# Optimization experiments

Hardware: AMD Instinct MI355X
Metric: run time of the kernel (lower is better)

## Reference

```python
import jax, jax.numpy as jnp
import numpy as np

V, D, R, E, B, T, S = 32000, 512, 512, 512, 32, 64, 64  # vocab, embed, rnn, enc, batch, trg_len, src_len


def setup_inputs() -> dict:
    key = jax.random.key(0)
    ks = jax.random.split(key, 16)
    s = 0.02
    return {
        "trg": jax.random.randint(ks[0], (B, T), 0, V),
        "enc_outputs": jax.random.normal(ks[1], (B, S, E), jnp.float32),
        "init_hidden": jax.random.normal(ks[2], (1, B, R), jnp.float32),
        "src_mask": jnp.ones((B, S), jnp.float32),
        "emb_W": jax.random.normal(ks[3], (V, D), jnp.float32) * s,   # embedding table, tied with logits weight
        "W_ih": jax.random.normal(ks[4], (3 * R, D + D), jnp.float32) * s,  # GRU input weights (input = emb + input_feed)
        "W_hh": jax.random.normal(ks[5], (3 * R, R), jnp.float32) * s,
        "b_ih": jnp.zeros((3 * R,), jnp.float32),
        "b_hh": jnp.zeros((3 * R,), jnp.float32),
        "W_a": jax.random.normal(ks[6], (R, E), jnp.float32) * s,     # attention 'general': enc_proj = enc @ W_a^T
        "W_h": jax.random.normal(ks[7], (D, R), jnp.float32) * s,     # outputs_fn='sum' projections to o_size=D
        "b_h": jnp.zeros((D,), jnp.float32),
        "W_c": jax.random.normal(ks[8], (D, E), jnp.float32) * s,
        "b_c": jnp.zeros((D,), jnp.float32),
        "b_logits": jnp.zeros((V,), jnp.float32),
    }


def _decode(trg, enc_outputs, init_hidden, src_mask, emb_W, W_ih, W_hh, b_ih, b_hh,
            W_a, W_h, b_h, W_c, b_c, b_logits):
    # teacher forcing (eval mode, sampling=0): input token at step i is trg[:, i]
    emb = emb_W[trg]                              # [B,T,D]
    enc_proj = jnp.einsum('bse,re->bsr', enc_outputs, W_a)  # precompute_enc_projections
    neg = jnp.asarray(-1e9, emb.dtype)

    def step(carry, e_i):
        h, o_prev = carry                          # h:[B,R], o_prev:[B,D] (input feed)
        x = jnp.concatenate([e_i, o_prev], -1)     # [B, 2D]
        gx = x @ W_ih.T + b_ih                     # [B, 3R]
        gh = h @ W_hh.T + b_hh
        gx_r, gx_z, gx_n = jnp.split(gx, 3, axis=-1)
        gh_r, gh_z, gh_n = jnp.split(gh, 3, axis=-1)
        r = jax.nn.sigmoid(gx_r + gh_r)
        z = jax.nn.sigmoid(gx_z + gh_z)
        n = jnp.tanh(gx_n + r * gh_n)
        h_new = (1.0 - z) * n + z * h              # GRU cell (torch gate order r,z,n)
        # attention ('general'): score = enc_proj . query
        scores = jnp.einsum('bsr,br->bs', enc_proj, h_new)
        scores = jnp.where(src_mask > 0, scores, neg)
        attn = jax.nn.softmax(scores, axis=-1)
        context = jnp.einsum('bs,bse->be', attn, enc_outputs)   # [B,E]
        o = jnp.tanh(h_new @ W_h.T + b_h + context @ W_c.T + b_c)  # sum + tanh
        logits = o @ emb_W.T + b_logits            # tied projection [B,V]
        return (h_new, o), logits

    h0 = init_hidden[0]                            # [B,R]
    o0 = jnp.zeros((B, emb_W.shape[1]), emb.dtype)
    _, logits = jax.lax.scan(step, (h0, o0), jnp.swapaxes(emb, 0, 1))
    return jnp.swapaxes(logits, 0, 1)              # [B,T,V]


def reference(trg, enc_outputs, init_hidden, src_mask, emb_W, W_ih, W_hh, b_ih, b_hh,
              W_a, W_h, b_h, W_c, b_c, b_logits):
    return _decode(trg, enc_outputs, init_hidden, src_mask, emb_W, W_ih, W_hh,
                   b_ih, b_hh, W_a, W_h, b_h, W_c, b_c, b_logits)
```

## Files before the change

kernel.cpp:

```cpp
#include <hip/hip_runtime.h>

#define V_ 32000
#define D_ 512
#define R_ 512
#define E_ 512
#define B_ 32
#define T_ 64
#define S_ 64
#define BT_ (B_ * T_)
#define G3_ (3 * R_)

typedef _Float16 f16;
typedef _Float16 f16x2 __attribute__((ext_vector_type(2)));
typedef _Float16 f16x8 __attribute__((ext_vector_type(8)));
typedef __bf16 bf16x8 __attribute__((ext_vector_type(8)));
typedef float f32x4 __attribute__((ext_vector_type(4)));

#define PAIR(v, i) (f16x2){(v)[2*(i)], (v)[2*(i)+1]}

__device__ __forceinline__ float fdot2_(f16x2 a, f16x2 b, float c) {
    return __builtin_amdgcn_fdot2(a, b, c, false);
}
__device__ __forceinline__ float sigmoidf_(float x) {
    return 1.0f / (1.0f + __expf(-x));
}

__global__ __launch_bounds__(256) void k_convert_bf16(const float* __restrict__ src,
                                                      __bf16* __restrict__ dst, int n8) {
    int i = blockIdx.x * 256 + threadIdx.x;
    if (i >= n8) return;
    float4 a = *(const float4*)&src[(size_t)i * 8];
    float4 b = *(const float4*)&src[(size_t)i * 8 + 4];
    bf16x8 o;
    o[0] = (__bf16)a.x; o[1] = (__bf16)a.y; o[2] = (__bf16)a.z; o[3] = (__bf16)a.w;
    o[4] = (__bf16)b.x; o[5] = (__bf16)b.y; o[6] = (__bf16)b.z; o[7] = (__bf16)b.w;
    *(bf16x8*)&dst[(size_t)i * 8] = o;
}

__global__ __launch_bounds__(256) void k_convert_f16(const float* __restrict__ src,
                                                     f16* __restrict__ dst, int n8) {
    int i = blockIdx.x * 256 + threadIdx.x;
    if (i >= n8) return;
    float4 a = *(const float4*)&src[(size_t)i * 8];
    float4 b = *(const float4*)&src[(size_t)i * 8 + 4];
    f16x8 o;
    o[0] = (f16)a.x; o[1] = (f16)a.y; o[2] = (f16)a.z; o[3] = (f16)a.w;
    o[4] = (f16)b.x; o[5] = (f16)b.y; o[6] = (f16)b.z; o[7] = (f16)b.w;
    *(f16x8*)&dst[(size_t)i * 8] = o;
}

__global__ __launch_bounds__(256) void k_gather_emb(const int* __restrict__ trg,
                                                    const __bf16* __restrict__ embW,
                                                    __bf16* __restrict__ dst) {
    int id = blockIdx.x * 256 + threadIdx.x;
    int bt = id >> 6, c = id & 63;
    int tok = trg[bt];
    *(uint4*)&dst[(size_t)bt * 512 + c * 8] = *(const uint4*)&embW[(size_t)tok * 512 + c * 8];
}

__global__ __launch_bounds__(256) void k_gemm_bf16(const __bf16* __restrict__ A,
                                                   const __bf16* __restrict__ B,
                                                   const float* __restrict__ bias,
                                                   float* __restrict__ out,
                                                   int M, int N, int K, int lda, int ldb,
                                                   int mode) {
    __shared__ __bf16 lA[128 * 40];
    __shared__ __bf16 lB[128 * 40];
    const int Mt = M >> 7;
    const int mt = blockIdx.x % Mt, nt = blockIdx.x / Mt;
    const int m0 = mt << 7, n0 = nt << 7;
    const int tid = threadIdx.x;
    const int w = tid >> 6, ln = tid & 63;
    const int wm = w >> 1, wn = w & 1;

    f32x4 acc[4][4];
#pragma unroll
    for (int mi = 0; mi < 4; ++mi)
#pragma unroll
        for (int ni = 0; ni < 4; ++ni) acc[mi][ni] = (f32x4){0.f, 0.f, 0.f, 0.f};

    const int k0 = (ln >> 4) * 8, rr = ln & 15;

    for (int kk = 0; kk < K; kk += 32) {
        __syncthreads();
#pragma unroll
        for (int p = 0; p < 2; ++p) {
            int i = p * 256 + tid;
            int r = i >> 2, q = i & 3;
            *(uint4*)&lA[r * 40 + q * 8] = *(const uint4*)&A[(size_t)(m0 + r) * lda + kk + q * 8];
            *(uint4*)&lB[r * 40 + q * 8] = *(const uint4*)&B[(size_t)(n0 + r) * ldb + kk + q * 8];
        }
        __syncthreads();
        bf16x8 af[4], bf[4];
#pragma unroll
        for (int mi = 0; mi < 4; ++mi) af[mi] = *(bf16x8*)&lA[(wm * 64 + mi * 16 + rr) * 40 + k0];
#pragma unroll
        for (int ni = 0; ni < 4; ++ni) bf[ni] = *(bf16x8*)&lB[(wn * 64 + ni * 16 + rr) * 40 + k0];
#pragma unroll
        for (int mi = 0; mi < 4; ++mi)
#pragma unroll
            for (int ni = 0; ni < 4; ++ni)
                acc[mi][ni] = __builtin_amdgcn_mfma_f32_16x16x32_bf16(af[mi], bf[ni], acc[mi][ni], 0, 0, 0);
    }

    const int rq = ln >> 4;
#pragma unroll
    for (int mi = 0; mi < 4; ++mi) {
#pragma unroll
        for (int ni = 0; ni < 4; ++ni) {
            int col = n0 + wn * 64 + ni * 16 + rr;
            float bv = bias ? bias[col] : 0.f;
#pragma unroll
            for (int reg = 0; reg < 4; ++reg) {
                int row = m0 + wm * 64 + mi * 16 + rq * 4 + reg;
                float v = acc[mi][ni][reg] + bv;
                if (mode == 0) {
                    out[(size_t)row * N + col] = v;
                } else {
                    int bb = row >> 6, tt = row & 63;
                    out[((size_t)tt * G3_ + col) * B_ + bb] = v;
                }
            }
        }
    }
}

__global__ __launch_bounds__(256) void k_pack_gates(const float* __restrict__ Wih,
                                                    const float* __restrict__ Whh,
                                                    f16* __restrict__ Wg) {
    int idx = blockIdx.x * 256 + threadIdx.x;
    int j3 = idx >> 10, k = idx & 1023;
    float v = (k < 512) ? Wih[(size_t)j3 * 1024 + 512 + k] : Whh[(size_t)j3 * 512 + (k - 512)];
    Wg[idx] = (f16)v;
}
__global__ __launch_bounds__(256) void k_pack_ewT(const float* __restrict__ ew, f16* __restrict__ ewT) {
    int idx = blockIdx.x * 256 + threadIdx.x;
    int b = idx >> 15, d = (idx >> 6) & 511, s = idx & 63;
    ewT[idx] = (f16)ew[((size_t)b * 64 + s) * 512 + d];
}
__global__ __launch_bounds__(256) void k_init_state(const float* __restrict__ init_h,
                                                    f16* __restrict__ x16,
                                                    float* __restrict__ hbuf) {
    int idx = blockIdx.x * 256 + threadIdx.x;
    int b = idx >> 10, k = idx & 1023;
    if (k < 512) {
        x16[idx] = (f16)0.f;
    } else {
        float v = init_h[(size_t)b * 512 + (k - 512)];
        x16[idx] = (f16)v;
        hbuf[(size_t)b * 512 + (k - 512)] = v;
    }
}

__global__ __launch_bounds__(256) void k_stepA(
    const f16* __restrict__ Wg, const float* __restrict__ gp, const float* __restrict__ bhh,
    const f16* __restrict__ x_in, f16* __restrict__ x_out,
    const float* __restrict__ h_in, float* __restrict__ h_out) {
    __shared__ __align__(16) f16 x2l[32 * 1032];
    const int tid = threadIdx.x;
    const int wgid = blockIdx.x;
    const int bA = tid & 31;
    const int half = (tid >> 5) & 1;
    const int jl = tid >> 6;
    const int j = wgid * 4 + jl;

#pragma unroll
    for (int i = 0; i < 16; ++i) {
        int f = tid + i * 256;
        int row = f >> 7, col = f & 127;
        *(uint4*)(x2l + row * 1032 + col * 8) = *(const uint4*)(x_in + (size_t)f * 8);
    }
    __syncthreads();

    const f16* xb = x2l + bA * 1032 + half * 512;
    const f16* wr = Wg + (size_t)(j) * 1024 + half * 512;
    const f16* wz = Wg + (size_t)(512 + j) * 1024 + half * 512;
    const f16* wn = Wg + (size_t)(1024 + j) * 1024 + half * 512;
    float ar = 0.f, az = 0.f, an = 0.f;
#pragma unroll 4
    for (int c = 0; c < 64; ++c) {
        f16x8 xv = *(const f16x8*)(xb + c * 8);
        f16x8 wrv = *(const f16x8*)(wr + c * 8);
        f16x8 wzv = *(const f16x8*)(wz + c * 8);
        f16x8 wnv = *(const f16x8*)(wn + c * 8);
#pragma unroll
        for (int q = 0; q < 4; ++q) {
            f16x2 xp = PAIR(xv, q);
            ar = fdot2_(xp, PAIR(wrv, q), ar);
            az = fdot2_(xp, PAIR(wzv, q), az);
            an = fdot2_(xp, PAIR(wnv, q), an);
        }
    }
    float aro = __shfl_xor(ar, 32);
    float azo = __shfl_xor(az, 32);
    float ano = __shfl_xor(an, 32);
    float gr = gp[(size_t)j * 32 + bA];
    float gz = gp[(size_t)(512 + j) * 32 + bA];
    float gn = gp[(size_t)(1024 + j) * 32 + bA];
    float rpre = gr + bhh[j] + ar + aro;
    float zpre = gz + bhh[512 + j] + az + azo;
    float r = sigmoidf_(rpre);
    float z = sigmoidf_(zpre);
    float gxn = gn + (half ? ano : an);
    float ghn = bhh[1024 + j] + (half ? an : ano);
    float n = tanhf(gxn + r * ghn);
    float hp = h_in[(size_t)bA * 512 + j];
    float hnew = (1.f - z) * n + z * hp;
    if (half == 0) {
        h_out[(size_t)bA * 512 + j] = hnew;
        x_out[(size_t)bA * 1024 + 512 + j] = (f16)hnew;
    }
}

__global__ __launch_bounds__(256) void k_stepB(
    const f16* __restrict__ whf16, const f16* __restrict__ epf16, const f16* __restrict__ encWcT,
    const float* __restrict__ mask, const float* __restrict__ bh, const float* __restrict__ bc,
    f16* __restrict__ x_out, __bf16* __restrict__ obf, int t) {
    __shared__ __align__(16) f16 hl16[512];
    __shared__ float sc_[64];
    __shared__ float s_af[64];
    __shared__ f16x2 a2l[32];
    const int tid = threadIdx.x;
    const int b = blockIdx.x >> 1, dh = blockIdx.x & 1;

    if (tid < 64) {
        *(uint4*)(hl16 + tid * 8) = *(const uint4*)(x_out + (size_t)b * 1024 + 512 + tid * 8);
    }
    __syncthreads();

    {
        int s = tid >> 2, q = tid & 3;
        const f16* ep = epf16 + ((size_t)(b * 64 + s)) * 512 + q * 128;
        const f16* hh = hl16 + q * 128;
        float a = 0.f;
#pragma unroll
        for (int c = 0; c < 16; ++c) {
            f16x8 ev = *(const f16x8*)(ep + c * 8);
            f16x8 xv = *(const f16x8*)(hh + c * 8);
#pragma unroll
            for (int qq = 0; qq < 4; ++qq) a = fdot2_(PAIR(ev, qq), PAIR(xv, qq), a);
        }
        a += __shfl_xor(a, 1);
        a += __shfl_xor(a, 2);
        if (q == 0) sc_[s] = a;
    }
    __syncthreads();
    if (tid < 64) {
        float s = sc_[tid];
        s = (mask[b * 64 + tid] > 0.f) ? s : -1e9f;
        float m = s;
#pragma unroll
        for (int d = 1; d < 64; d <<= 1) m = fmaxf(m, __shfl_xor(m, d));
        float e = __expf(s - m);
        float sum = e;
#pragma unroll
        for (int d = 1; d < 64; d <<= 1) sum += __shfl_xor(sum, d);
        s_af[tid] = e / sum;
    }
    __syncthreads();
    if (tid < 32) {
        a2l[tid] = (f16x2){(f16)s_af[2 * tid], (f16)s_af[2 * tid + 1]};
    }
    __syncthreads();
    {
        const int d = dh * 256 + tid;
        float u = bh[d] + bc[d];
        const f16* wrow = whf16 + (size_t)d * 512;
#pragma unroll 8
        for (int c = 0; c < 64; ++c) {
            f16x8 wv = *(const f16x8*)(wrow + c * 8);
            f16x8 xv = *(const f16x8*)(hl16 + c * 8);
#pragma unroll
            for (int qq = 0; qq < 4; ++qq) u = fdot2_(PAIR(wv, qq), PAIR(xv, qq), u);
        }
        const f16* ew = encWcT + ((size_t)b * 512 + d) * 64;
#pragma unroll
        for (int c = 0; c < 8; ++c) {
            f16x8 ev = *(const f16x8*)(ew + c * 8);
#pragma unroll
            for (int qq = 0; qq < 4; ++qq) u = fdot2_(PAIR(ev, qq), a2l[c * 4 + qq], u);
        }
        float o = tanhf(u);
        obf[((size_t)b * 64 + t) * 512 + d] = (__bf16)o;
        x_out[(size_t)b * 1024 + d] = (f16)o;
    }
}

extern "C" void kernel_launch(void* const* d_in, const int* in_sizes, int n_in,
                              void* d_out, int out_size, void* d_ws, size_t ws_size,
                              hipStream_t stream) {
    const int* trg = (const int*)d_in[0];
    const float* enc = (const float*)d_in[1];
    const float* init_h = (const float*)d_in[2];
    const float* mask = (const float*)d_in[3];
    const float* embW = (const float*)d_in[4];
    const float* Wih = (const float*)d_in[5];
    const float* Whh = (const float*)d_in[6];
    const float* bih = (const float*)d_in[7];
    const float* bhh = (const float*)d_in[8];
    const float* Wa = (const float*)d_in[9];
    const float* Wh = (const float*)d_in[10];
    const float* bh = (const float*)d_in[11];
    const float* Wc = (const float*)d_in[12];
    const float* bc = (const float*)d_in[13];
    const float* blog = (const float*)d_in[14];
    float* out = (float*)d_out;

    char* w = (char*)d_ws;
    auto alloc = [&](size_t bytes) { char* p = w; w += (bytes + 255) & ~(size_t)255; return p; };
    __bf16* embW_bf = (__bf16*)alloc((size_t)V_ * D_ * 2);
    __bf16* Wih_bf  = (__bf16*)alloc((size_t)G3_ * 1024 * 2);
    __bf16* Wa_bf   = (__bf16*)alloc((size_t)R_ * E_ * 2);
    __bf16* Wc_bf   = (__bf16*)alloc((size_t)D_ * E_ * 2);
    __bf16* enc_bf  = (__bf16*)alloc((size_t)BT_ * E_ * 2);
    __bf16* emb_bf  = (__bf16*)alloc((size_t)BT_ * D_ * 2);
    float* gxe      = (float*)alloc((size_t)T_ * G3_ * B_ * 4);
    float* encproj  = (float*)alloc((size_t)BT_ * R_ * 4);
    float* encWc    = (float*)alloc((size_t)BT_ * D_ * 4);
    f16* Wg         = (f16*)alloc((size_t)G3_ * 1024 * 2);
    f16* whf16      = (f16*)alloc((size_t)512 * 512 * 2);
    f16* epf16      = (f16*)alloc((size_t)BT_ * 512 * 2);
    f16* encWcT     = (f16*)alloc((size_t)32 * 512 * 64 * 2);
    f16* x16        = (f16*)alloc((size_t)2 * 32 * 1024 * 2);
    float* hbuf     = (float*)alloc((size_t)2 * 32 * 512 * 4);
    __bf16* o_bf    = (__bf16*)alloc((size_t)BT_ * D_ * 2);

    k_convert_bf16<<<(V_ * D_ / 8 + 255) / 256, 256, 0, stream>>>(embW, embW_bf, V_ * D_ / 8);
    k_convert_bf16<<<(G3_ * 1024 / 8 + 255) / 256, 256, 0, stream>>>(Wih, Wih_bf, G3_ * 1024 / 8);
    k_convert_bf16<<<(R_ * E_ / 8 + 255) / 256, 256, 0, stream>>>(Wa, Wa_bf, R_ * E_ / 8);
    k_convert_bf16<<<(D_ * E_ / 8 + 255) / 256, 256, 0, stream>>>(Wc, Wc_bf, D_ * E_ / 8);
    k_convert_bf16<<<(BT_ * E_ / 8 + 255) / 256, 256, 0, stream>>>(enc, enc_bf, BT_ * E_ / 8);

    k_gather_emb<<<(BT_ * 64) / 256, 256, 0, stream>>>(trg, embW_bf, emb_bf);

    k_gemm_bf16<<<(BT_ / 128) * (G3_ / 128), 256, 0, stream>>>(
        emb_bf, Wih_bf, bih, gxe, BT_, G3_, 512, 512, 1024, 1);

    k_gemm_bf16<<<(BT_ / 128) * (R_ / 128), 256, 0, stream>>>(
        enc_bf, Wa_bf, nullptr, encproj, BT_, R_, 512, 512, 512, 0);
    k_gemm_bf16<<<(BT_ / 128) * (D_ / 128), 256, 0, stream>>>(
        enc_bf, Wc_bf, nullptr, encWc, BT_, D_, 512, 512, 512, 0);

    k_pack_gates<<<(G3_ * 1024) / 256, 256, 0, stream>>>(Wih, Whh, Wg);
    k_convert_f16<<<(512 * 512 / 8 + 255) / 256, 256, 0, stream>>>(Wh, whf16, 512 * 512 / 8);
    k_convert_f16<<<(BT_ * 512 / 8 + 255) / 256, 256, 0, stream>>>(encproj, epf16, BT_ * 512 / 8);
    k_pack_ewT<<<(32 * 512 * 64) / 256, 256, 0, stream>>>(encWc, encWcT);
    k_init_state<<<(32 * 1024) / 256, 256, 0, stream>>>(init_h, x16, hbuf);

    for (int t = 0; t < T_; ++t) {
        const f16* x_in = x16 + (size_t)(t & 1) * 32 * 1024;
        f16* x_out = x16 + (size_t)((t + 1) & 1) * 32 * 1024;
        const float* h_in = hbuf + (size_t)(t & 1) * 32 * 512;
        float* h_out = hbuf + (size_t)((t + 1) & 1) * 32 * 512;
        k_stepA<<<128, 256, 0, stream>>>(Wg, gxe + (size_t)t * G3_ * B_, bhh,
                                         x_in, x_out, h_in, h_out);
        k_stepB<<<64, 256, 0, stream>>>(whf16, epf16, encWcT, mask, bh, bc,
                                        x_out, o_bf, t);
    }

    k_gemm_bf16<<<(BT_ / 128) * (V_ / 128), 256, 0, stream>>>(
        o_bf, embW_bf, blog, out, BT_, V_, 512, 512, 512, 0);
}
```

Measured before the change: 1.613 ms.

## Fuse setup conversions into one kernel, gather embeddings in GEMM, use direct-to-LDS loads

```diff
diff --git a/kernel.cpp b/kernel.cpp
--- a/kernel.cpp
+++ b/kernel.cpp
@@ -18,6 +18,9 @@
 
 #define PAIR(v, i) (f16x2){(v)[2*(i)], (v)[2*(i)+1]}
 
+typedef __attribute__((address_space(3))) char lds_char;
+typedef __attribute__((address_space(1))) const char glob_char;
+
 __device__ __forceinline__ float fdot2_(f16x2 a, f16x2 b, float c) {
     return __builtin_amdgcn_fdot2(a, b, c, false);
 }
@@ -25,47 +28,91 @@
     return 1.0f / (1.0f + __expf(-x));
 }
 
-__global__ __launch_bounds__(256) void k_convert_bf16(const float* __restrict__ src,
-                                                      __bf16* __restrict__ dst, int n8) {
-    int i = blockIdx.x * 256 + threadIdx.x;
-    if (i >= n8) return;
-    float4 a = *(const float4*)&src[(size_t)i * 8];
-    float4 b = *(const float4*)&src[(size_t)i * 8 + 4];
+#define SN0 ((size_t)V_ * D_)
+#define SN1 ((size_t)G3_ * 512)
+#define SN2 ((size_t)BT_ * E_)
+#define SN3 ((size_t)1024 * 512)
+#define SN4 ((size_t)G3_ * 1024)
+#define SN5 ((size_t)512 * 512)
+#define SN6 ((size_t)32 * 1024)
+
+__device__ __forceinline__ void cvt8_bf16(const float* s, __bf16* d) {
+    float4 a = *(const float4*)s, b = *(const float4*)(s + 4);
     bf16x8 o;
     o[0] = (__bf16)a.x; o[1] = (__bf16)a.y; o[2] = (__bf16)a.z; o[3] = (__bf16)a.w;
     o[4] = (__bf16)b.x; o[5] = (__bf16)b.y; o[6] = (__bf16)b.z; o[7] = (__bf16)b.w;
-    *(bf16x8*)&dst[(size_t)i * 8] = o;
-}
-
-__global__ __launch_bounds__(256) void k_convert_f16(const float* __restrict__ src,
-                                                     f16* __restrict__ dst, int n8) {
-    int i = blockIdx.x * 256 + threadIdx.x;
-    if (i >= n8) return;
-    float4 a = *(const float4*)&src[(size_t)i * 8];
-    float4 b = *(const float4*)&src[(size_t)i * 8 + 4];
+    *(bf16x8*)d = o;
+}
+__device__ __forceinline__ void cvt8_f16(const float* s, f16* d) {
+    float4 a = *(const float4*)s, b = *(const float4*)(s + 4);
     f16x8 o;
     o[0] = (f16)a.x; o[1] = (f16)a.y; o[2] = (f16)a.z; o[3] = (f16)a.w;
     o[4] = (f16)b.x; o[5] = (f16)b.y; o[6] = (f16)b.z; o[7] = (f16)b.w;
-    *(f16x8*)&dst[(size_t)i * 8] = o;
-}
-
-__global__ __launch_bounds__(256) void k_gather_emb(const int* __restrict__ trg,
-                                                    const __bf16* __restrict__ embW,
-                                                    __bf16* __restrict__ dst) {
-    int id = blockIdx.x * 256 + threadIdx.x;
-    int bt = id >> 6, c = id & 63;
-    int tok = trg[bt];
-    *(uint4*)&dst[(size_t)bt * 512 + c * 8] = *(const uint4*)&embW[(size_t)tok * 512 + c * 8];
+    *(f16x8*)d = o;
+}
+
+__global__ __launch_bounds__(256) void k_setup(
+    const float* __restrict__ embW, const float* __restrict__ Wih,
+    const float* __restrict__ Whh, const float* __restrict__ enc,
+    const float* __restrict__ Wa, const float* __restrict__ Wc,
+    const float* __restrict__ Wh, const float* __restrict__ init_h,
+    __bf16* __restrict__ embW_bf, __bf16* __restrict__ Wih_bf,
+    __bf16* __restrict__ enc_bf, __bf16* __restrict__ Wab_bf,
+    f16* __restrict__ Wg, f16* __restrict__ whf16,
+    f16* __restrict__ x16, float* __restrict__ hbuf) {
+    size_t e = ((size_t)blockIdx.x * 256 + threadIdx.x) * 8;
+    if (e < SN0) { cvt8_bf16(embW + e, embW_bf + e); return; }
+    e -= SN0;
+    if (e < SN1) {
+        size_t j3 = e >> 9, k = e & 511;
+        cvt8_bf16(Wih + j3 * 1024 + k, Wih_bf + e);
+        return;
+    }
+    e -= SN1;
+    if (e < SN2) { cvt8_bf16(enc + e, enc_bf + e); return; }
+    e -= SN2;
+    if (e < SN3) {
+        size_t r = e >> 9, k = e & 511;
+        const float* s = (r < 512) ? (Wa + r * 512 + k) : (Wc + (r - 512) * 512 + k);
+        cvt8_bf16(s, Wab_bf + e);
+        return;
+    }
+    e -= SN3;
+    if (e < SN4) {
+        size_t j3 = e >> 10, k = e & 1023;
+        const float* s = (k < 512) ? (Wih + j3 * 1024 + 512 + k) : (Whh + j3 * 512 + (k - 512));
+        cvt8_f16(s, Wg + e);
+        return;
+    }
+    e -= SN4;
+    if (e < SN5) { cvt8_f16(Wh + e, whf16 + e); return; }
+    e -= SN5;
+    if (e < SN6) {
+        size_t b = e >> 10, k = e & 1023;
+        if (k < 512) {
+            f16x8 z = {(f16)0.f, (f16)0.f, (f16)0.f, (f16)0.f,
+                       (f16)0.f, (f16)0.f, (f16)0.f, (f16)0.f};
+            *(f16x8*)(x16 + e) = z;
+        } else {
+            const float* s = init_h + b * 512 + (k - 512);
+            cvt8_f16(s, x16 + e);
+            *(float4*)(hbuf + b * 512 + (k - 512)) = *(const float4*)s;
+            *(float4*)(hbuf + b * 512 + (k - 512) + 4) = *(const float4*)(s + 4);
+        }
+    }
 }
 
 __global__ __launch_bounds__(256) void k_gemm_bf16(const __bf16* __restrict__ A,
-                                                   const __bf16* __restrict__ B,
+                                                   const __bf16* __restrict__ Bm,
                                                    const float* __restrict__ bias,
                                                    float* __restrict__ out,
+                                                   f16* __restrict__ out16a,
+                                                   f16* __restrict__ out16b,
+                                                   const int* __restrict__ trg,
                                                    int M, int N, int K, int lda, int ldb,
                                                    int mode) {
-    __shared__ __bf16 lA[128 * 40];
-    __shared__ __bf16 lB[128 * 40];
+    __shared__ __bf16 lA[128 * 32];
+    __shared__ __bf16 lB[128 * 32];
     const int Mt = M >> 7;
     const int mt = blockIdx.x % Mt, nt = blockIdx.x / Mt;
     const int m0 = mt << 7, n0 = nt << 7;
@@ -73,6 +120,15 @@
     const int w = tid >> 6, ln = tid & 63;
     const int wm = w >> 1, wn = w & 1;
 
+    int arow[2], brow[2];
+#pragma unroll
+    for (int h = 0; h < 2; ++h) {
+        int r = h * 64 + w * 16 + (ln >> 2);
+        arow[h] = trg ? trg[m0 + r] : (m0 + r);
+        brow[h] = n0 + r;
+    }
+    const int q8 = (ln & 3) * 8;
+
     f32x4 acc[4][4];
 #pragma unroll
     for (int mi = 0; mi < 4; ++mi)
@@ -84,18 +140,20 @@
     for (int kk = 0; kk < K; kk += 32) {
         __syncthreads();
 #pragma unroll
-        for (int p = 0; p < 2; ++p) {
-            int i = p * 256 + tid;
-            int r = i >> 2, q = i & 3;
-            *(uint4*)&lA[r * 40 + q * 8] = *(const uint4*)&A[(size_t)(m0 + r) * lda + kk + q * 8];
-            *(uint4*)&lB[r * 40 + q * 8] = *(const uint4*)&B[(size_t)(n0 + r) * ldb + kk + q * 8];
+        for (int h = 0; h < 2; ++h) {
+            const __bf16* srcA = A + (size_t)arow[h] * lda + kk + q8;
+            const __bf16* srcB = Bm + (size_t)brow[h] * ldb + kk + q8;
+            __bf16* dstA = lA + (size_t)(h * 64 + w * 16) * 32;
+            __bf16* dstB = lB + (size_t)(h * 64 + w * 16) * 32;
+            __builtin_amdgcn_global_load_lds((glob_char*)srcA, (lds_char*)dstA, 16, 0, 0);
+            __builtin_amdgcn_global_load_lds((glob_char*)srcB, (lds_char*)dstB, 16, 0, 0);
         }
         __syncthreads();
         bf16x8 af[4], bf[4];
 #pragma unroll
-        for (int mi = 0; mi < 4; ++mi) af[mi] = *(bf16x8*)&lA[(wm * 64 + mi * 16 + rr) * 40 + k0];
-#pragma unroll
-        for (int ni = 0; ni < 4; ++ni) bf[ni] = *(bf16x8*)&lB[(wn * 64 + ni * 16 + rr) * 40 + k0];
+        for (int mi = 0; mi < 4; ++mi) af[mi] = *(bf16x8*)&lA[(wm * 64 + mi * 16 + rr) * 32 + k0];
+#pragma unroll
+        for (int ni = 0; ni < 4; ++ni) bf[ni] = *(bf16x8*)&lB[(wn * 64 + ni * 16 + rr) * 32 + k0];
 #pragma unroll
         for (int mi = 0; mi < 4; ++mi)
 #pragma unroll
@@ -116,39 +174,18 @@
                 float v = acc[mi][ni][reg] + bv;
                 if (mode == 0) {
                     out[(size_t)row * N + col] = v;
-                } else {
+                } else if (mode == 1) {
                     int bb = row >> 6, tt = row & 63;
                     out[((size_t)tt * G3_ + col) * B_ + bb] = v;
+                } else {
+                    if (col < 512) {
+                        out16a[(size_t)row * 512 + col] = (f16)v;
+                    } else {
+                        out16b[(((size_t)(row >> 6) * 512 + (col - 512)) << 6) | (row & 63)] = (f16)v;
+                    }
                 }
             }
         }
-    }
-}
-
-__global__ __launch_bounds__(256) void k_pack_gates(const float* __restrict__ Wih,
-                                                    const float* __restrict__ Whh,
-                                                    f16* __restrict__ Wg) {
-    int idx = blockIdx.x * 256 + threadIdx.x;
-    int j3 = idx >> 10, k = idx & 1023;
-    float v = (k < 512) ? Wih[(size_t)j3 * 1024 + 512 + k] : Whh[(size_t)j3 * 512 + (k - 512)];
-    Wg[idx] = (f16)v;
-}
-__global__ __launch_bounds__(256) void k_pack_ewT(const float* __restrict__ ew, f16* __restrict__ ewT) {
-    int idx = blockIdx.x * 256 + threadIdx.x;
-    int b = idx >> 15, d = (idx >> 6) & 511, s = idx & 63;
-    ewT[idx] = (f16)ew[((size_t)b * 64 + s) * 512 + d];
-}
-__global__ __launch_bounds__(256) void k_init_state(const float* __restrict__ init_h,
-                                                    f16* __restrict__ x16,
-                                                    float* __restrict__ hbuf) {
-    int idx = blockIdx.x * 256 + threadIdx.x;
-    int b = idx >> 10, k = idx & 1023;
-    if (k < 512) {
-        x16[idx] = (f16)0.f;
-    } else {
-        float v = init_h[(size_t)b * 512 + (k - 512)];
-        x16[idx] = (f16)v;
-        hbuf[(size_t)b * 512 + (k - 512)] = v;
     }
 }
 
@@ -308,44 +345,32 @@
 
     char* w = (char*)d_ws;
     auto alloc = [&](size_t bytes) { char* p = w; w += (bytes + 255) & ~(size_t)255; return p; };
-    __bf16* embW_bf = (__bf16*)alloc((size_t)V_ * D_ * 2);
-    __bf16* Wih_bf  = (__bf16*)alloc((size_t)G3_ * 1024 * 2);
-    __bf16* Wa_bf   = (__bf16*)alloc((size_t)R_ * E_ * 2);
-    __bf16* Wc_bf   = (__bf16*)alloc((size_t)D_ * E_ * 2);
-    __bf16* enc_bf  = (__bf16*)alloc((size_t)BT_ * E_ * 2);
-    __bf16* emb_bf  = (__bf16*)alloc((size_t)BT_ * D_ * 2);
+    __bf16* embW_bf = (__bf16*)alloc(SN0 * 2);
+    __bf16* Wih_bf  = (__bf16*)alloc(SN1 * 2);
+    __bf16* enc_bf  = (__bf16*)alloc(SN2 * 2);
+    __bf16* Wab_bf  = (__bf16*)alloc(SN3 * 2);
+    f16* Wg         = (f16*)alloc(SN4 * 2);
+    f16* whf16      = (f16*)alloc(SN5 * 2);
     float* gxe      = (float*)alloc((size_t)T_ * G3_ * B_ * 4);
-    float* encproj  = (float*)alloc((size_t)BT_ * R_ * 4);
-    float* encWc    = (float*)alloc((size_t)BT_ * D_ * 4);
-    f16* Wg         = (f16*)alloc((size_t)G3_ * 1024 * 2);
-    f16* whf16      = (f16*)alloc((size_t)512 * 512 * 2);
     f16* epf16      = (f16*)alloc((size_t)BT_ * 512 * 2);
     f16* encWcT     = (f16*)alloc((size_t)32 * 512 * 64 * 2);
     f16* x16        = (f16*)alloc((size_t)2 * 32 * 1024 * 2);
     float* hbuf     = (float*)alloc((size_t)2 * 32 * 512 * 4);
     __bf16* o_bf    = (__bf16*)alloc((size_t)BT_ * D_ * 2);
 
-    k_convert_bf16<<<(V_ * D_ / 8 + 255) / 256, 256, 0, stream>>>(embW, embW_bf, V_ * D_ / 8);
-    k_convert_bf16<<<(G3_ * 1024 / 8 + 255) / 256, 256, 0, stream>>>(Wih, Wih_bf, G3_ * 1024 / 8);
-    k_convert_bf16<<<(R_ * E_ / 8 + 255) / 256, 256, 0, stream>>>(Wa, Wa_bf, R_ * E_ / 8);
-    k_convert_bf16<<<(D_ * E_ / 8 + 255) / 256, 256, 0, stream>>>(Wc, Wc_bf, D_ * E_ / 8);
-    k_convert_bf16<<<(BT_ * E_ / 8 + 255) / 256, 256, 0, stream>>>(enc, enc_bf, BT_ * E_ / 8);
-
-    k_gather_emb<<<(BT_ * 64) / 256, 256, 0, stream>>>(trg, embW_bf, emb_bf);
+    {
+        size_t total8 = (SN0 + SN1 + SN2 + SN3 + SN4 + SN5 + SN6) / 8;
+        int wgs = (int)((total8 + 255) / 256);
+        k_setup<<<wgs, 256, 0, stream>>>(embW, Wih, Whh, enc, Wa, Wc, Wh, init_h,
+                                         embW_bf, Wih_bf, enc_bf, Wab_bf, Wg, whf16,
+                                         x16, hbuf);
+    }
 
     k_gemm_bf16<<<(BT_ / 128) * (G3_ / 128), 256, 0, stream>>>(
-        emb_bf, Wih_bf, bih, gxe, BT_, G3_, 512, 512, 1024, 1);
-
-    k_gemm_bf16<<<(BT_ / 128) * (R_ / 128), 256, 0, stream>>>(
-        enc_bf, Wa_bf, nullptr, encproj, BT_, R_, 512, 512, 512, 0);
-    k_gemm_bf16<<<(BT_ / 128) * (D_ / 128), 256, 0, stream>>>(
-        enc_bf, Wc_bf, nullptr, encWc, BT_, D_, 512, 512, 512, 0);
-
-    k_pack_gates<<<(G3_ * 1024) / 256, 256, 0, stream>>>(Wih, Whh, Wg);
-    k_convert_f16<<<(512 * 512 / 8 + 255) / 256, 256, 0, stream>>>(Wh, whf16, 512 * 512 / 8);
-    k_convert_f16<<<(BT_ * 512 / 8 + 255) / 256, 256, 0, stream>>>(encproj, epf16, BT_ * 512 / 8);
-    k_pack_ewT<<<(32 * 512 * 64) / 256, 256, 0, stream>>>(encWc, encWcT);
-    k_init_state<<<(32 * 1024) / 256, 256, 0, stream>>>(init_h, x16, hbuf);
+        embW_bf, Wih_bf, bih, gxe, nullptr, nullptr, trg, BT_, G3_, 512, 512, 512, 1);
+
+    k_gemm_bf16<<<(BT_ / 128) * (1024 / 128), 256, 0, stream>>>(
+        enc_bf, Wab_bf, nullptr, nullptr, epf16, encWcT, nullptr, BT_, 1024, 512, 512, 512, 2);
 
     for (int t = 0; t < T_; ++t) {
         const f16* x_in = x16 + (size_t)(t & 1) * 32 * 1024;
@@ -359,5 +384,5 @@
     }
 
     k_gemm_bf16<<<(BT_ / 128) * (V_ / 128), 256, 0, stream>>>(
-        o_bf, embW_bf, blog, out, BT_, V_, 512, 512, 512, 0);
-}
+        o_bf, embW_bf, blog, out, nullptr, nullptr, nullptr, BT_, V_, 512, 512, 512, 0);
+}
```

Result: faster. 1.576 ms (-2.3%).
